# Performance work log

Hardware: AMD Instinct MI355X
Metric: run time of the kernel (lower is better)

The kernel has to match this reference:

```python
import jax, jax.numpy as jnp
import numpy as np

B, C, T, F = 16, 64, 400, 64
H = C          # GRU hidden == numUnits == channel
G = 8          # PE groups


def _gru(xs, Wih, Whh, bih, bhh):
    """PyTorch-style GRU, batch_first. xs: [N, T, I]; Wih: [3H, I]; Whh: [3H, H]."""
    gx = jnp.einsum('nti,gi->ntg', xs, Wih) + bih          # [N, T, 3H] input gates precomputed
    Hh = Whh.shape[1]

    def step(h, gxt):
        gh = h @ Whh.T + bhh                               # [N, 3H]
        xr, xz, xn = jnp.split(gxt, 3, axis=-1)
        hr, hz, hn = jnp.split(gh, 3, axis=-1)
        r = jax.nn.sigmoid(xr + hr)
        z = jax.nn.sigmoid(xz + hz)
        n = jnp.tanh(xn + r * hn)
        hn_new = (1.0 - z) * n + z * h
        return hn_new, hn_new

    h0 = jnp.zeros((xs.shape[0], Hh), xs.dtype)
    _, ys = jax.lax.scan(step, h0, jnp.swapaxes(gx, 0, 1))
    return jnp.swapaxes(ys, 0, 1)                          # [N, T, H]


def _ln2(x, g, b, eps=1e-8):
    """LayerNorm over last two dims [width, numUnits]."""
    mu = x.mean(axis=(-2, -1), keepdims=True)
    var = x.var(axis=(-2, -1), keepdims=True)
    return (x - mu) / jnp.sqrt(var + eps) * g + b


def setup_inputs() -> dict:
    key = jax.random.key(0)
    ks = jax.random.split(key, 24)
    s = 0.1

    def rn(k, shape):
        return jax.random.normal(k, shape, dtype=jnp.float32) * s

    return {
        'x': jax.random.normal(ks[0], (B, C, T, F), dtype=jnp.float32),
        # intra bidirectional GRU (input = C = H)
        'intra_Wih_f': rn(ks[1], (3 * H, H)), 'intra_Whh_f': rn(ks[2], (3 * H, H)),
        'intra_bih_f': rn(ks[3], (3 * H,)),   'intra_bhh_f': rn(ks[4], (3 * H,)),
        'intra_Wih_b': rn(ks[5], (3 * H, H)), 'intra_Whh_b': rn(ks[6], (3 * H, H)),
        'intra_bih_b': rn(ks[7], (3 * H,)),   'intra_bhh_b': rn(ks[8], (3 * H,)),
        'intra_fc_W': rn(ks[9], (H, 2 * H)),  'intra_fc_b': rn(ks[10], (H,)),
        'intra_ln_g': jnp.ones((F, H), jnp.float32), 'intra_ln_b': jnp.zeros((F, H), jnp.float32),
        # PE: 8 grouped GRUs + FCs (stacked along group axis)
        'pe_Wih': rn(ks[11], (G, 3 * H, H)), 'pe_Whh': rn(ks[12], (G, 3 * H, H)),
        'pe_bih': rn(ks[13], (G, 3 * H)),    'pe_bhh': rn(ks[14], (G, 3 * H)),
        'pe_fc_W': rn(ks[15], (G, H, H)),    'pe_fc_b': rn(ks[16], (G, H)),
        'pe_ln_g': jnp.ones((F, H), jnp.float32), 'pe_ln_b': jnp.zeros((F, H), jnp.float32),
    }


def _forward(x, intra_Wih_f, intra_Whh_f, intra_bih_f, intra_bhh_f,
             intra_Wih_b, intra_Whh_b, intra_bih_b, intra_bhh_b,
             intra_fc_W, intra_fc_b, intra_ln_g, intra_ln_b,
             pe_Wih, pe_Whh, pe_bih, pe_bhh, pe_fc_W, pe_fc_b, pe_ln_g, pe_ln_b):
    b, c, t, f = x.shape
    xp = jnp.transpose(x, (0, 2, 3, 1))                    # [b, t, f, c]

    # ---- intra path: bidirectional GRU along frequency f ----
    seq = xp.reshape(b * t, f, c)
    fwd = _gru(seq, intra_Wih_f, intra_Whh_f, intra_bih_f, intra_bhh_f)
    bwd = jnp.flip(_gru(jnp.flip(seq, 1), intra_Wih_b, intra_Whh_b, intra_bih_b, intra_bhh_b), 1)
    intra = jnp.concatenate([fwd, bwd], axis=-1) @ intra_fc_W.T + intra_fc_b
    intra = _ln2(intra.reshape(b, t, f, c), intra_ln_g, intra_ln_b)
    intra_out = xp + intra                                  # residual

    # ---- PE: 8 grouped GRUs along time t ----
    y = jnp.transpose(intra_out, (0, 2, 1, 3))             # [b, f, t, c]
    fg = f // G
    yg = y.reshape(b, G, fg, t, c)                         # chunk freq into G groups
    yg = jnp.transpose(yg, (1, 0, 2, 3, 4)).reshape(G, b * fg, t, c)
    rnn = jax.vmap(_gru)(yg, pe_Wih, pe_Whh, pe_bih, pe_bhh)    # [G, b*fg, t, H]
    fc = jnp.einsum('gnth,goh->gnto', rnn, pe_fc_W) + pe_fc_b[:, None, None, :]
    fc = fc.reshape(G, b, fg, t, H).transpose(1, 0, 2, 3, 4).reshape(b, f, t, H)
    inter = _ln2(jnp.transpose(fc, (0, 2, 1, 3)), pe_ln_g, pe_ln_b)   # [b, t, f, c]

    out = intra + inter                                     # note: residual with intra (pre-add), per source
    return jnp.transpose(out, (0, 3, 1, 2))                 # [b, c, t, f]


def reference(x, intra_Wih_f, intra_Whh_f, intra_bih_f, intra_bhh_f,
              intra_Wih_b, intra_Whh_b, intra_bih_b, intra_bhh_b,
              intra_fc_W, intra_fc_b, intra_ln_g, intra_ln_b,
              pe_Wih, pe_Whh, pe_bih, pe_bhh, pe_fc_W, pe_fc_b, pe_ln_g, pe_ln_b):
    return _forward(x, intra_Wih_f, intra_Whh_f, intra_bih_f, intra_bhh_f,
                    intra_Wih_b, intra_Whh_b, intra_bih_b, intra_bhh_b,
                    intra_fc_W, intra_fc_b, intra_ln_g, intra_ln_b,
                    pe_Wih, pe_Whh, pe_bih, pe_bhh, pe_fc_W, pe_fc_b, pe_ln_g, pe_ln_b)
```

## Files before the change

### kernel.cpp

```cpp
#include <hip/hip_runtime.h>
#include <hip/hip_bf16.h>

typedef unsigned short u16;
typedef __attribute__((ext_vector_type(8))) short short8;
typedef __attribute__((ext_vector_type(4))) float f32x4;

#define MFMA16(A,B,C) __builtin_amdgcn_mfma_f32_16x16x32_bf16((A),(B),(C),0,0,0)

__device__ __forceinline__ float bf2f(u16 u){ return __uint_as_float(((unsigned)u)<<16); }
__device__ __forceinline__ u16 f2bf(float f){
  unsigned x = __float_as_uint(f);
  return (u16)((x + 0x7FFFu + ((x>>16)&1u)) >> 16);
}
__device__ __forceinline__ float sigm(float x){ return __fdividef(1.f, 1.f + __expf(-x)); }
__device__ __forceinline__ float tanh_(float x){ return __fdividef(2.f, 1.f + __expf(-2.f*x)) - 1.f; }
__device__ __forceinline__ short8 ldg8(const u16* p){ return *(const short8*)p; }

struct CvtArgs {
  const void* src[21];
  u16* dst[21];
  int n[21];
};

__global__ __launch_bounds__(256,1) void k_cvt(CvtArgs a)
{
  const u16* d = (const u16*)a.src[0];
  int imp = 0, pl = 0;
#pragma unroll
  for (int i = 0; i < 128; i += 2){
    u16 u = d[i]; int e = (u >> 7) & 0xFF;
    if (u){ if (e >= 104 && e <= 134) pl++; else imp++; }
  }
  bool isf32 = imp > pl;

  int which, i0, stride;
  if (blockIdx.x < 20){ which = blockIdx.x + 1; i0 = threadIdx.x; stride = 256; }
  else { which = 0; i0 = (blockIdx.x - 20)*256 + threadIdx.x; stride = (gridDim.x - 20)*256; }
  int n = a.n[which];
  u16* dst = a.dst[which];
  if (isf32){
    const float* s = (const float*)a.src[which];
    for (int i = i0; i < n; i += stride) dst[i] = f2bf(s[i]);
  } else {
    const u16* s = (const u16*)a.src[which];
    for (int i = i0; i < n; i += stride) dst[i] = s[i];
  }
}

__global__ __launch_bounds__(256,1) void k_transpose(const u16* __restrict__ x, u16* __restrict__ xp)
{
  int nb = blockIdx.x; int b = nb/400, t = nb - b*400;
  int tid = threadIdx.x;
  __shared__ u16 tl[64*66];
  int f0 = (tid & 31) * 2;
#pragma unroll
  for (int p = 0; p < 8; p++){
    int c = p*8 + (tid>>5);
    unsigned u = *(const unsigned*)(x + (((size_t)b*64 + c)*400 + t)*64 + f0);
    *(unsigned*)(tl + c*66 + f0) = u;
  }
  __syncthreads();
  int c0 = (tid & 31) * 2;
  u16* dst = xp + (size_t)nb*4096;
#pragma unroll
  for (int p = 0; p < 8; p++){
    int f = p*8 + (tid>>5);
    unsigned u = (unsigned)tl[c0*66 + f] | ((unsigned)tl[(c0+1)*66 + f] << 16);
    *(unsigned*)(dst + f*64 + c0) = u;
  }
}

__global__ __launch_bounds__(64,1) void k_intra(
    const u16* __restrict__ xp,
    const u16* __restrict__ Wih_f, const u16* __restrict__ Whh_f,
    const u16* __restrict__ bih_f, const u16* __restrict__ bhh_f,
    const u16* __restrict__ Wih_b, const u16* __restrict__ Whh_b,
    const u16* __restrict__ bih_b, const u16* __restrict__ bhh_b,
    u16* __restrict__ yfo, u16* __restrict__ ybo)
{
  int blk = blockIdx.x;
  int dir = blk >= 400;
  int tile = dir ? blk - 400 : blk;
  int n0 = tile * 16;
  const u16* Wih = dir ? Wih_b : Wih_f;
  const u16* Whh = dir ? Whh_b : Whh_f;
  const u16* bih = dir ? bih_b : bih_f;
  const u16* bhh = dir ? bhh_b : bhh_f;
  u16* yo = dir ? ybo : yfo;

  int lane = threadIdx.x;
  int m = lane & 15, q = lane >> 4;

  short8 wrx[4][2], wzx[4][2], wnx[4][2], wrh[4][2], wzh[4][2], wnh[4][2];
#pragma unroll
  for (int nt = 0; nt < 4; nt++){
#pragma unroll
    for (int kc = 0; kc < 2; kc++){
      int co = kc*32 + q*8;
      wrx[nt][kc] = ldg8(Wih + (      nt*16 + m)*64 + co);
      wzx[nt][kc] = ldg8(Wih + ( 64 + nt*16 + m)*64 + co);
      wnx[nt][kc] = ldg8(Wih + (128 + nt*16 + m)*64 + co);
      wrh[nt][kc] = ldg8(Whh + (      nt*16 + m)*64 + co);
      wzh[nt][kc] = ldg8(Whh + ( 64 + nt*16 + m)*64 + co);
      wnh[nt][kc] = ldg8(Whh + (128 + nt*16 + m)*64 + co);
    }
  }
  float br[4], bz[4], bnx_[4], bnh_[4];
#pragma unroll
  for (int nt = 0; nt < 4; nt++){
    int u = nt*16 + m;
    br[nt]   = bf2f(bih[u])     + bf2f(bhh[u]);
    bz[nt]   = bf2f(bih[64+u])  + bf2f(bhh[64+u]);
    bnx_[nt] = bf2f(bih[128+u]);
    bnh_[nt] = bf2f(bhh[128+u]);
  }

  __shared__ u16 hl[16*72];
  float h[4][4];
#pragma unroll
  for (int nt=0;nt<4;nt++){
#pragma unroll
    for (int p=0;p<4;p++) h[nt][p] = 0.f;
  }
  short8 hf0 = {0,0,0,0,0,0,0,0}, hf1 = {0,0,0,0,0,0,0,0};
  int f = dir ? 63 : 0, df = dir ? -1 : 1;
  short8 xf0 = ldg8(xp + ((size_t)(n0+m)*64 + f)*64 + q*8);
  short8 xf1 = ldg8(xp + ((size_t)(n0+m)*64 + f)*64 + 32 + q*8);

  for (int s = 0; s < 64; s++){
    f32x4 ar[4], az[4], anx[4], anh[4];
#pragma unroll
    for (int nt=0;nt<4;nt++){
      ar[nt]  = (f32x4){br[nt],br[nt],br[nt],br[nt]};
      az[nt]  = (f32x4){bz[nt],bz[nt],bz[nt],bz[nt]};
      anx[nt] = (f32x4){bnx_[nt],bnx_[nt],bnx_[nt],bnx_[nt]};
      anh[nt] = (f32x4){bnh_[nt],bnh_[nt],bnh_[nt],bnh_[nt]};
    }
#pragma unroll
    for (int nt=0;nt<4;nt++){
      ar[nt]  = MFMA16(hf0, wrh[nt][0], ar[nt]);
      ar[nt]  = MFMA16(hf1, wrh[nt][1], ar[nt]);
      ar[nt]  = MFMA16(xf0, wrx[nt][0], ar[nt]);
      ar[nt]  = MFMA16(xf1, wrx[nt][1], ar[nt]);
      az[nt]  = MFMA16(hf0, wzh[nt][0], az[nt]);
      az[nt]  = MFMA16(hf1, wzh[nt][1], az[nt]);
      az[nt]  = MFMA16(xf0, wzx[nt][0], az[nt]);
      az[nt]  = MFMA16(xf1, wzx[nt][1], az[nt]);
      anx[nt] = MFMA16(xf0, wnx[nt][0], anx[nt]);
      anx[nt] = MFMA16(xf1, wnx[nt][1], anx[nt]);
      anh[nt] = MFMA16(hf0, wnh[nt][0], anh[nt]);
      anh[nt] = MFMA16(hf1, wnh[nt][1], anh[nt]);
    }
    int fn = f + df;
    if (s < 63){
      xf0 = ldg8(xp + ((size_t)(n0+m)*64 + fn)*64 + q*8);
      xf1 = ldg8(xp + ((size_t)(n0+m)*64 + fn)*64 + 32 + q*8);
    }
#pragma unroll
    for (int nt=0;nt<4;nt++){
#pragma unroll
      for (int p=0;p<4;p++){
        float r  = sigm(ar[nt][p]);
        float z  = sigm(az[nt][p]);
        float n  = tanh_(anx[nt][p] + r*anh[nt][p]);
        float hn = n + z*(h[nt][p] - n);
        h[nt][p] = hn;
        hl[(q*4+p)*72 + nt*16 + m] = f2bf(hn);
      }
    }
    __threadfence_block();
    int sl = lane >> 2, ch = lane & 3;
    short8 y0 = *(const short8*)(hl + sl*72 + ch*16);
    short8 y1 = *(const short8*)(hl + sl*72 + ch*16 + 8);
    *(short8*)(yo + ((size_t)(n0+sl)*64 + f)*64 + ch*16)     = y0;
    *(short8*)(yo + ((size_t)(n0+sl)*64 + f)*64 + ch*16 + 8) = y1;
    hf0 = *(const short8*)(hl + m*72 + q*8);
    hf1 = *(const short8*)(hl + m*72 + 32 + q*8);
    __threadfence_block();
    f = fn;
  }
}

__global__ __launch_bounds__(256,1) void k_ifc(
  const u16* __restrict__ yf, const u16* __restrict__ yb,
  const u16* __restrict__ fcw, const u16* __restrict__ fcb,
  const u16* __restrict__ lng, const u16* __restrict__ lnb,
  const u16* __restrict__ xp, u16* __restrict__ lnI, u16* __restrict__ iout)
{
  int nb = blockIdx.x; int b = nb/400, t = nb - b*400;
  int tid = threadIdx.x; int wv = tid>>6; int lane = tid&63;
  int m = lane&15, q = lane>>4;
  int rb = nb*64 + wv*16;
  short8 a0 = ldg8(yf + (size_t)(rb+m)*64 + q*8);
  short8 a1 = ldg8(yf + (size_t)(rb+m)*64 + 32 + q*8);
  short8 a2 = ldg8(yb + (size_t)(rb+m)*64 + q*8);
  short8 a3 = ldg8(yb + (size_t)(rb+m)*64 + 32 + q*8);
  f32x4 acc[4];
#pragma unroll
  for (int nt=0;nt<4;nt++){
    float bias = bf2f(fcb[nt*16+m]);
    acc[nt] = (f32x4){bias,bias,bias,bias};
    acc[nt] = MFMA16(a0, ldg8(fcw + (nt*16+m)*128 +      q*8), acc[nt]);
    acc[nt] = MFMA16(a1, ldg8(fcw + (nt*16+m)*128 + 32 + q*8), acc[nt]);
    acc[nt] = MFMA16(a2, ldg8(fcw + (nt*16+m)*128 + 64 + q*8), acc[nt]);
    acc[nt] = MFMA16(a3, ldg8(fcw + (nt*16+m)*128 + 96 + q*8), acc[nt]);
  }
  float s=0.f, s2=0.f;
#pragma unroll
  for (int nt=0;nt<4;nt++){
#pragma unroll
    for (int p=0;p<4;p++){ float v=acc[nt][p]; s+=v; s2+=v*v; }
  }
  for (int o=32;o>0;o>>=1){ s += __shfl_down(s,o); s2 += __shfl_down(s2,o); }
  __shared__ float red[8];
  if (lane==0){ red[wv]=s; red[4+wv]=s2; }
  __syncthreads();
  float S  = red[0]+red[1]+red[2]+red[3];
  float S2 = red[4]+red[5]+red[6]+red[7];
  float mu = S*(1.f/4096.f);
  float rstd = rsqrtf(S2*(1.f/4096.f) - mu*mu + 1e-8f);
#pragma unroll
  for (int nt=0;nt<4;nt++){
#pragma unroll
    for (int p=0;p<4;p++){
      int row = wv*16 + q*4 + p;
      int col = nt*16 + m;
      float v = (acc[nt][p]-mu)*rstd;
      v = v*bf2f(lng[row*64+col]) + bf2f(lnb[row*64+col]);
      lnI[(size_t)nb*4096 + row*64 + col] = f2bf(v);
      float xv = bf2f(xp[(size_t)nb*4096 + row*64 + col]);
      iout[(((size_t)b*64 + row)*400 + t)*64 + col] = f2bf(v + xv);
    }
  }
}

__global__ __launch_bounds__(64,1) void k_gx(const u16* __restrict__ io,
   const u16* __restrict__ pw, const u16* __restrict__ pb, u16* __restrict__ gx)
{
  int r0 = blockIdx.x * 16;
  int seq = r0 / 400;
  int g = (seq & 63) >> 3;
  int lane = threadIdx.x; int m = lane&15, q = lane>>4;
  short8 a0 = ldg8(io + (size_t)(r0+m)*64 + q*8);
  short8 a1 = ldg8(io + (size_t)(r0+m)*64 + 32 + q*8);
  const u16* W = pw + g*12288;
#pragma unroll
  for (int nt=0; nt<12; nt++){
    float bias = bf2f(pb[g*192 + nt*16 + m]);
    f32x4 acc = (f32x4){bias,bias,bias,bias};
    acc = MFMA16(a0, ldg8(W + (nt*16+m)*64 + q*8), acc);
    acc = MFMA16(a1, ldg8(W + (nt*16+m)*64 + 32 + q*8), acc);
#pragma unroll
    for (int p=0;p<4;p++)
      gx[(size_t)(r0 + q*4 + p)*192 + nt*16 + m] = f2bf(acc[p]);
  }
}

__global__ __launch_bounds__(64,1) void k_pe(const u16* __restrict__ gx,
  const u16* __restrict__ whh, const u16* __restrict__ bhh, u16* __restrict__ ype)
{
  int seq = blockIdx.x;
  int g = (seq & 63) >> 3;
  int j = threadIdx.x;
  const u16* W = whh + g*12288;
  float wr[64], wz[64], wn[64];
#pragma unroll
  for (int kk=0; kk<8; kk++){
    short8 vr = ldg8(W + (      j)*64 + kk*8);
    short8 vz = ldg8(W + ( 64 + j)*64 + kk*8);
    short8 vn = ldg8(W + (128 + j)*64 + kk*8);
#pragma unroll
    for (int i=0;i<8;i++){
      wr[kk*8+i] = bf2f((u16)vr[i]);
      wz[kk*8+i] = bf2f((u16)vz[i]);
      wn[kk*8+i] = bf2f((u16)vn[i]);
    }
  }
  float brh = bf2f(bhh[g*192 + j]);
  float bzh = bf2f(bhh[g*192 + 64 + j]);
  float bnh = bf2f(bhh[g*192 + 128 + j]);
  float h = 0.f;
  const u16* gp = gx + (size_t)seq*400*192;
  u16* yp = ype + (size_t)seq*400*64 + j;
  for (int t = 0; t < 400; t++){
    float xr = bf2f(gp[j]), xz = bf2f(gp[64+j]), xn = bf2f(gp[128+j]);
    float ar = brh, az = bzh, an = bnh;
#pragma unroll
    for (int k = 0; k < 64; k++){
      float hk = __int_as_float(__builtin_amdgcn_readlane(__float_as_int(h), k));
      ar = fmaf(hk, wr[k], ar);
      az = fmaf(hk, wz[k], az);
      an = fmaf(hk, wn[k], an);
    }
    float r = sigm(xr + ar);
    float z = sigm(xz + az);
    float n = tanh_(xn + r*an);
    h = n + z*(h - n);
    *yp = f2bf(h);
    gp += 192; yp += 64;
  }
}

__global__ __launch_bounds__(64,1) void k_pefc(const u16* __restrict__ ype,
  const u16* __restrict__ fw, const u16* __restrict__ fb, u16* __restrict__ fcpe)
{
  int r0 = blockIdx.x * 16;
  int seq = r0 / 400;
  int g = (seq & 63) >> 3;
  int b = seq >> 6, f = seq & 63;
  int tb = r0 - seq*400;
  int lane = threadIdx.x; int m = lane&15, q = lane>>4;
  short8 a0 = ldg8(ype + (size_t)(r0+m)*64 + q*8);
  short8 a1 = ldg8(ype + (size_t)(r0+m)*64 + 32 + q*8);
  const u16* W = fw + g*4096;
#pragma unroll
  for (int nt=0;nt<4;nt++){
    float bias = bf2f(fb[g*64 + nt*16 + m]);
    f32x4 acc = (f32x4){bias,bias,bias,bias};
    acc = MFMA16(a0, ldg8(W + (nt*16+m)*64 + q*8), acc);
    acc = MFMA16(a1, ldg8(W + (nt*16+m)*64 + 32 + q*8), acc);
#pragma unroll
    for (int p=0;p<4;p++){
      int t = tb + q*4 + p;
      fcpe[(((size_t)b*400 + t)*64 + f)*64 + nt*16 + m] = f2bf(acc[p]);
    }
  }
}

__global__ __launch_bounds__(256,1) void k_final(const u16* __restrict__ fcpe,
  const u16* __restrict__ lnI, const u16* __restrict__ g_, const u16* __restrict__ b_,
  float* __restrict__ out)
{
  int nb = blockIdx.x; int b = nb/400, t = nb - b*400;
  int tid = threadIdx.x;
  const u16* src = fcpe + (size_t)nb*4096 + tid*16;
  short8 v0 = ldg8(src), v1 = ldg8(src + 8);
  float v[16];
#pragma unroll
  for (int i=0;i<8;i++){ v[i] = bf2f((u16)v0[i]); v[8+i] = bf2f((u16)v1[i]); }
  float s=0.f, s2=0.f;
#pragma unroll
  for (int i=0;i<16;i++){ s+=v[i]; s2+=v[i]*v[i]; }
  int lane = tid&63, wv = tid>>6;
  for (int o=32;o>0;o>>=1){ s += __shfl_down(s,o); s2 += __shfl_down(s2,o); }
  __shared__ float red[8];
  __shared__ float tr[64*68];
  if (lane==0){ red[wv]=s; red[4+wv]=s2; }
  __syncthreads();
  float S  = red[0]+red[1]+red[2]+red[3];
  float S2 = red[4]+red[5]+red[6]+red[7];
  float mu = S*(1.f/4096.f);
  float rstd = rsqrtf(S2*(1.f/4096.f) - mu*mu + 1e-8f);
  int ff = tid>>2; int c0 = (tid&3)*16;
  const u16* lp = lnI + (size_t)nb*4096 + tid*16;
  short8 l0 = ldg8(lp), l1 = ldg8(lp + 8);
#pragma unroll
  for (int i=0;i<16;i++){
    int c = c0 + i;
    float x = (v[i]-mu)*rstd*bf2f(g_[ff*64+c]) + bf2f(b_[ff*64+c]);
    x += (i<8) ? bf2f((u16)l0[i]) : bf2f((u16)l1[i-8]);
    tr[c*68 + ff] = x;
  }
  __syncthreads();
  int cc = tid>>2, fc = (tid&3)*16;
  float* dst = out + (((size_t)b*64 + cc)*400 + t)*64 + fc;
#pragma unroll
  for (int i=0;i<16;i+=4){
    *(f32x4*)(dst + i) = *(const f32x4*)(tr + cc*68 + fc + i);
  }
}

extern "C" void kernel_launch(void* const* d_in, const int* in_sizes, int n_in,
                              void* d_out, int out_size, void* d_ws, size_t ws_size,
                              hipStream_t stream)
{
  (void)in_sizes; (void)n_in; (void)out_size; (void)ws_size;

  char* ws = (char*)d_ws;
  u16* xp   = (u16*)(ws + 0ull);
  u16* xb   = (u16*)(ws + 52428800ull);
  u16* yf   = (u16*)(ws + 52428800ull);
  u16* yb   = (u16*)(ws + 104857600ull);
  u16* lnI  = (u16*)(ws + 157286400ull);
  u16* iout = (u16*)(ws + 209715200ull);
  u16* gx   = (u16*)(ws + 0ull);
  u16* ype  = (u16*)(ws + 209715200ull);
  u16* fcpe = (u16*)(ws + 0ull);
  u16* wb   = (u16*)(ws + 262144000ull);

  static const int wn[21] = {26214400,
    12288,12288,192,192, 12288,12288,192,192,
    8192,64,4096,4096, 98304,98304,1536,1536, 32768,512,4096,4096};
  int woff[21]; woff[0] = 0;
  int acc = 0;
  for (int i = 1; i <= 20; i++){ woff[i] = acc; acc += wn[i]; }

  CvtArgs ca;
  for (int i = 0; i < 21; i++){
    ca.src[i] = d_in[i];
    ca.n[i] = wn[i];
    ca.dst[i] = (i == 0) ? xb : (wb + woff[i]);
  }

  const u16* iWihf = wb + woff[1];
  const u16* iWhhf = wb + woff[2];
  const u16* ibihf = wb + woff[3];
  const u16* ibhhf = wb + woff[4];
  const u16* iWihb = wb + woff[5];
  const u16* iWhhb = wb + woff[6];
  const u16* ibihb = wb + woff[7];
  const u16* ibhhb = wb + woff[8];
  const u16* fcW   = wb + woff[9];
  const u16* fcB   = wb + woff[10];
  const u16* ilng  = wb + woff[11];
  const u16* ilnb  = wb + woff[12];
  const u16* peWih = wb + woff[13];
  const u16* peWhh = wb + woff[14];
  const u16* pebih = wb + woff[15];
  const u16* pebhh = wb + woff[16];
  const u16* pefcW = wb + woff[17];
  const u16* pefcb = wb + woff[18];
  const u16* pelng = wb + woff[19];
  const u16* pelnb = wb + woff[20];

  k_cvt<<<dim3(2068), dim3(256), 0, stream>>>(ca);
  k_transpose<<<dim3(6400), dim3(256), 0, stream>>>(xb, xp);
  k_intra<<<dim3(800), dim3(64), 0, stream>>>(xp, iWihf, iWhhf, ibihf, ibhhf,
                                              iWihb, iWhhb, ibihb, ibhhb, yf, yb);
  k_ifc<<<dim3(6400), dim3(256), 0, stream>>>(yf, yb, fcW, fcB, ilng, ilnb, xp, lnI, iout);
  k_gx<<<dim3(25600), dim3(64), 0, stream>>>(iout, peWih, pebih, gx);
  k_pe<<<dim3(1024), dim3(64), 0, stream>>>(gx, peWhh, pebhh, ype);
  k_pefc<<<dim3(25600), dim3(64), 0, stream>>>(ype, pefcW, pefcb, fcpe);
  k_final<<<dim3(6400), dim3(256), 0, stream>>>(fcpe, lnI, pelng, pelnb, (float*)d_out);
}
```

Baseline: 1.267 ms.

## Batch 16 PE GRU sequences per block and compute recurrence with MFMA

The PE GRU recurrence kernel is rewritten so each block of four waves processes 16 sequences of one group together. The hidden-state matvec becomes a bf16 MFMA using a hi/lo split of h for extra precision. The new hidden state is exchanged through double-buffered LDS and the next step's input gates are prefetched. This replaces the per-sequence 64-thread scalar FMA loop with readlane broadcasts. The cost is only 64 blocks on a many-CU device, plus a block barrier every timestep.

Measured after the change: 1.249 ms. Within noise of the previous version (-1.4%).

```diff
diff --git a/kernel.cpp b/kernel.cpp
--- a/kernel.cpp
+++ b/kernel.cpp
@@ -4,6 +4,7 @@
 typedef unsigned short u16;
 typedef __attribute__((ext_vector_type(8))) short short8;
 typedef __attribute__((ext_vector_type(4))) float f32x4;
+typedef __attribute__((ext_vector_type(4))) unsigned short us4;
 
 #define MFMA16(A,B,C) __builtin_amdgcn_mfma_f32_16x16x32_bf16((A),(B),(C),0,0,0)
 
@@ -256,48 +257,99 @@
   }
 }
 
-__global__ __launch_bounds__(64,1) void k_pe(const u16* __restrict__ gx,
+__global__ __launch_bounds__(256,1) void k_pe(const u16* __restrict__ gx,
   const u16* __restrict__ whh, const u16* __restrict__ bhh, u16* __restrict__ ype)
 {
-  int seq = blockIdx.x;
-  int g = (seq & 63) >> 3;
-  int j = threadIdx.x;
+  int tile = blockIdx.x;
+  int g = tile >> 3, tl = tile & 7;
+  int tid = threadIdx.x;
+  int w = tid >> 6;
+  int lane = tid & 63;
+  int m = lane & 15, q = lane >> 4;
+
   const u16* W = whh + g*12288;
-  float wr[64], wz[64], wn[64];
-#pragma unroll
-  for (int kk=0; kk<8; kk++){
-    short8 vr = ldg8(W + (      j)*64 + kk*8);
-    short8 vz = ldg8(W + ( 64 + j)*64 + kk*8);
-    short8 vn = ldg8(W + (128 + j)*64 + kk*8);
-#pragma unroll
-    for (int i=0;i<8;i++){
-      wr[kk*8+i] = bf2f((u16)vr[i]);
-      wz[kk*8+i] = bf2f((u16)vz[i]);
-      wn[kk*8+i] = bf2f((u16)vn[i]);
-    }
-  }
-  float brh = bf2f(bhh[g*192 + j]);
-  float bzh = bf2f(bhh[g*192 + 64 + j]);
-  float bnh = bf2f(bhh[g*192 + 128 + j]);
-  float h = 0.f;
-  const u16* gp = gx + (size_t)seq*400*192;
-  u16* yp = ype + (size_t)seq*400*64 + j;
+  short8 wr[2], wz[2], wn[2];
+#pragma unroll
+  for (int kc = 0; kc < 2; kc++){
+    int co = kc*32 + q*8;
+    wr[kc] = ldg8(W + (((size_t)w    *16 + m))*64 + co);
+    wz[kc] = ldg8(W + (((size_t)(w+4)*16 + m))*64 + co);
+    wn[kc] = ldg8(W + (((size_t)(w+8)*16 + m))*64 + co);
+  }
+  float brh = bf2f(bhh[g*192 +       w*16 + m]);
+  float bzh = bf2f(bhh[g*192 + 64  + w*16 + m]);
+  float bnh = bf2f(bhh[g*192 + 128 + w*16 + m]);
+
+  const u16* bp[4];
+#pragma unroll
+  for (int p = 0; p < 4; p++){
+    int sl = q*4 + p;
+    int sidx = tl*16 + sl;
+    int seqg = (sidx >> 3)*64 + g*8 + (sidx & 7);
+    bp[p] = gx + (size_t)seqg*400*192 + w*16 + m;
+  }
+
+  int sls = w*4 + (lane >> 4);
+  int sidxs = tl*16 + sls;
+  int seqs_ = (sidxs >> 3)*64 + g*8 + (sidxs & 7);
+  int u0 = (lane & 15)*4;
+  u16* yp = ype + (size_t)seqs_*400*64 + u0;
+  int hlr = sls*72 + u0;
+
+  __shared__ u16 hl[2][2][16*72];
+
+  float hprev[4] = {0.f, 0.f, 0.f, 0.f};
+  short8 hA0 = {0,0,0,0,0,0,0,0}, hA1 = {0,0,0,0,0,0,0,0};
+  short8 hB0 = {0,0,0,0,0,0,0,0}, hB1 = {0,0,0,0,0,0,0,0};
+
+  u16 gr[4], gz[4], gn[4];
+#pragma unroll
+  for (int p = 0; p < 4; p++){ gr[p] = bp[p][0]; gz[p] = bp[p][64]; gn[p] = bp[p][128]; }
+
+  int cur = 0;
   for (int t = 0; t < 400; t++){
-    float xr = bf2f(gp[j]), xz = bf2f(gp[64+j]), xn = bf2f(gp[128+j]);
-    float ar = brh, az = bzh, an = bnh;
-#pragma unroll
-    for (int k = 0; k < 64; k++){
-      float hk = __int_as_float(__builtin_amdgcn_readlane(__float_as_int(h), k));
-      ar = fmaf(hk, wr[k], ar);
-      az = fmaf(hk, wz[k], az);
-      an = fmaf(hk, wn[k], an);
-    }
-    float r = sigm(xr + ar);
-    float z = sigm(xz + az);
-    float n = tanh_(xn + r*an);
-    h = n + z*(h - n);
-    *yp = f2bf(h);
-    gp += 192; yp += 64;
+    f32x4 ar, az, anh;
+    float gnf[4];
+#pragma unroll
+    for (int p = 0; p < 4; p++){
+      ar[p]  = bf2f(gr[p]) + brh;
+      az[p]  = bf2f(gz[p]) + bzh;
+      anh[p] = bnh;
+      gnf[p] = bf2f(gn[p]);
+    }
+    if (t < 399){
+#pragma unroll
+      for (int p = 0; p < 4; p++){
+        bp[p] += 192;
+        gr[p] = bp[p][0]; gz[p] = bp[p][64]; gn[p] = bp[p][128];
+      }
+    }
+    ar  = MFMA16(hA0, wr[0], ar);  ar  = MFMA16(hA1, wr[1], ar);
+    ar  = MFMA16(hB0, wr[0], ar);  ar  = MFMA16(hB1, wr[1], ar);
+    az  = MFMA16(hA0, wz[0], az);  az  = MFMA16(hA1, wz[1], az);
+    az  = MFMA16(hB0, wz[0], az);  az  = MFMA16(hB1, wz[1], az);
+    anh = MFMA16(hA0, wn[0], anh); anh = MFMA16(hA1, wn[1], anh);
+    anh = MFMA16(hB0, wn[0], anh); anh = MFMA16(hB1, wn[1], anh);
+#pragma unroll
+    for (int p = 0; p < 4; p++){
+      float r  = sigm(ar[p]);
+      float z  = sigm(az[p]);
+      float n  = tanh_(gnf[p] + r*anh[p]);
+      float hn = n + z*(hprev[p] - n);
+      hprev[p] = hn;
+      u16 hi = f2bf(hn);
+      int off = (q*4 + p)*72 + w*16 + m;
+      hl[cur][0][off] = hi;
+      hl[cur][1][off] = f2bf(hn - bf2f(hi));
+    }
+    __syncthreads();
+    *(us4*)yp = *(const us4*)&hl[cur][0][hlr];
+    yp += 64;
+    hA0 = *(const short8*)&hl[cur][0][m*72 + q*8];
+    hA1 = *(const short8*)&hl[cur][0][m*72 + 32 + q*8];
+    hB0 = *(const short8*)&hl[cur][1][m*72 + q*8];
+    hB1 = *(const short8*)&hl[cur][1][m*72 + 32 + q*8];
+    cur ^= 1;
   }
 }
 
@@ -429,7 +481,7 @@
                                               iWihb, iWhhb, ibihb, ibhhb, yf, yb);
   k_ifc<<<dim3(6400), dim3(256), 0, stream>>>(yf, yb, fcW, fcB, ilng, ilnb, xp, lnI, iout);
   k_gx<<<dim3(25600), dim3(64), 0, stream>>>(iout, peWih, pebih, gx);
-  k_pe<<<dim3(1024), dim3(64), 0, stream>>>(gx, peWhh, pebhh, ype);
+  k_pe<<<dim3(64), dim3(256), 0, stream>>>(gx, peWhh, pebhh, ype);
   k_pefc<<<dim3(25600), dim3(64), 0, stream>>>(ype, pefcW, pefcb, fcpe);
   k_final<<<dim3(6400), dim3(256), 0, stream>>>(fcpe, lnI, pelng, pelnb, (float*)d_out);
 }
```

## Compute PE GRU recurrence with bf16 MFMA and split hi/lo hidden state

Applied to the files above, without the earlier changes.

Replaces the scalar per-lane FMA loop over readlane-broadcast hidden values in the grouped GRU kernel with matrix-core MFMA instructions. Each step computes the hidden-to-gate products from bf16 weight fragments held in registers. The hidden state is split into bf16 high and low parts to keep near-fp32 accuracy, and is exchanged through LDS each step. Input-gate values are now prefetched two steps ahead. The aim is to cut the serial per-step VALU work, at the cost of bf16 recurrent weights, redundant MFMA rows and an LDS round trip on the critical path.

Result: no change. 1.273 ms (+0.5%).

```diff
diff --git a/kernel.cpp b/kernel.cpp
--- a/kernel.cpp
+++ b/kernel.cpp
@@ -261,44 +261,106 @@
 {
   int seq = blockIdx.x;
   int g = (seq & 63) >> 3;
-  int j = threadIdx.x;
-  const u16* W = whh + g*12288;
-  float wr[64], wz[64], wn[64];
-#pragma unroll
-  for (int kk=0; kk<8; kk++){
-    short8 vr = ldg8(W + (      j)*64 + kk*8);
-    short8 vz = ldg8(W + ( 64 + j)*64 + kk*8);
-    short8 vn = ldg8(W + (128 + j)*64 + kk*8);
-#pragma unroll
-    for (int i=0;i<8;i++){
-      wr[kk*8+i] = bf2f((u16)vr[i]);
-      wz[kk*8+i] = bf2f((u16)vz[i]);
-      wn[kk*8+i] = bf2f((u16)vn[i]);
-    }
-  }
-  float brh = bf2f(bhh[g*192 + j]);
-  float bzh = bf2f(bhh[g*192 + 64 + j]);
-  float bnh = bf2f(bhh[g*192 + 128 + j]);
+  int lane = threadIdx.x;
+  int m = lane & 15, q = lane >> 4;
+
+  const u16* W = whh + (size_t)g*12288;
+  short8 wr[4][2], wz[4][2], wn[4][2];
+#pragma unroll
+  for (int nt = 0; nt < 4; nt++){
+#pragma unroll
+    for (int kc = 0; kc < 2; kc++){
+      int co = kc*32 + q*8;
+      wr[nt][kc] = ldg8(W + (      nt*16 + m)*64 + co);
+      wz[nt][kc] = ldg8(W + ( 64 + nt*16 + m)*64 + co);
+      wn[nt][kc] = ldg8(W + (128 + nt*16 + m)*64 + co);
+    }
+  }
+  float br_[4], bz_[4], bn_[4];
+#pragma unroll
+  for (int nt = 0; nt < 4; nt++){
+    br_[nt] = bf2f(bhh[g*192 +       nt*16 + m]);
+    bz_[nt] = bf2f(bhh[g*192 + 64  + nt*16 + m]);
+    bn_[nt] = bf2f(bhh[g*192 + 128 + nt*16 + m]);
+  }
+
+  const u16* gp = gx + (size_t)seq*400*192 + lane;
+  u16* yp = ype + (size_t)seq*400*64 + lane;
+
+  u16 cr0 = gp[0],   cz0 = gp[64],  cn0 = gp[128];
+  u16 cr1 = gp[192], cz1 = gp[256], cn1 = gp[320];
+  gp += 384;
+
+  __shared__ __align__(16) u16 hbuf[128];
+
   float h = 0.f;
-  const u16* gp = gx + (size_t)seq*400*192;
-  u16* yp = ype + (size_t)seq*400*64 + j;
-  for (int t = 0; t < 400; t++){
-    float xr = bf2f(gp[j]), xz = bf2f(gp[64+j]), xn = bf2f(gp[128+j]);
-    float ar = brh, az = bzh, an = bnh;
-#pragma unroll
-    for (int k = 0; k < 64; k++){
-      float hk = __int_as_float(__builtin_amdgcn_readlane(__float_as_int(h), k));
-      ar = fmaf(hk, wr[k], ar);
-      az = fmaf(hk, wz[k], az);
-      an = fmaf(hk, wn[k], an);
-    }
-    float r = sigm(xr + ar);
-    float z = sigm(xz + az);
-    float n = tanh_(xn + r*an);
-    h = n + z*(h - n);
-    *yp = f2bf(h);
-    gp += 192; yp += 64;
-  }
+  short8 ah0 = {0,0,0,0,0,0,0,0}, ah1 = {0,0,0,0,0,0,0,0};
+  short8 al0 = {0,0,0,0,0,0,0,0}, al1 = {0,0,0,0,0,0,0,0};
+
+  f32x4 accr[4], accz[4], accn[4];
+#pragma unroll
+  for (int nt=0; nt<4; nt++){
+    accr[nt] = (f32x4){br_[nt],br_[nt],br_[nt],br_[nt]};
+    accz[nt] = (f32x4){bz_[nt],bz_[nt],bz_[nt],bz_[nt]};
+    accn[nt] = (f32x4){bn_[nt],bn_[nt],bn_[nt],bn_[nt]};
+  }
+
+#define PE_STEP(CR, CZ, CN, PFOFF, COND)                                      \
+  {                                                                           \
+    float xr = bf2f(CR), xz = bf2f(CZ), xn = bf2f(CN);                        \
+    if (COND){ CR = gp[PFOFF]; CZ = gp[(PFOFF)+64]; CN = gp[(PFOFF)+128]; }   \
+    \
+    \
+    _Pragma("unroll")                                                         \
+    for (int nt=0; nt<4; nt++){                                               \
+      accr[nt][0] = br_[nt]; accz[nt][0] = bz_[nt]; accn[nt][0] = bn_[nt];    \
+    }                                                                         \
+    _Pragma("unroll")                                                         \
+    for (int nt=0; nt<4; nt++){                                               \
+      accr[nt] = MFMA16(ah0, wr[nt][0], accr[nt]);                            \
+      accr[nt] = MFMA16(ah1, wr[nt][1], accr[nt]);                            \
+      accr[nt] = MFMA16(al0, wr[nt][0], accr[nt]);                            \
+      accr[nt] = MFMA16(al1, wr[nt][1], accr[nt]);                            \
+      accz[nt] = MFMA16(ah0, wz[nt][0], accz[nt]);                            \
+      accz[nt] = MFMA16(ah1, wz[nt][1], accz[nt]);                            \
+      accz[nt] = MFMA16(al0, wz[nt][0], accz[nt]);                            \
+      accz[nt] = MFMA16(al1, wz[nt][1], accz[nt]);                            \
+      accn[nt] = MFMA16(ah0, wn[nt][0], accn[nt]);                            \
+      accn[nt] = MFMA16(ah1, wn[nt][1], accn[nt]);                            \
+      accn[nt] = MFMA16(al0, wn[nt][0], accn[nt]);                            \
+      accn[nt] = MFMA16(al1, wn[nt][1], accn[nt]);                            \
+    }                                                                         \
+         \
+    float ar = accr[0][0]; float az = accz[0][0]; float an = accn[0][0];      \
+    ar = (q==1) ? accr[1][0] : ar; az = (q==1) ? accz[1][0] : az;             \
+    an = (q==1) ? accn[1][0] : an;                                            \
+    ar = (q==2) ? accr[2][0] : ar; az = (q==2) ? accz[2][0] : az;             \
+    an = (q==2) ? accn[2][0] : an;                                            \
+    ar = (q==3) ? accr[3][0] : ar; az = (q==3) ? accz[3][0] : az;             \
+    an = (q==3) ? accn[3][0] : an;                                            \
+    float r = sigm(xr + ar);                                                  \
+    float z = sigm(xz + az);                                                  \
+    float n = tanh_(xn + r*an);                                               \
+    h = n + z*(h - n);                                                        \
+    u16 hi = f2bf(h);                                                         \
+    u16 lo = f2bf(h - bf2f(hi));                                              \
+    *yp = hi; yp += 64;                                                       \
+    hbuf[lane] = hi;                                                          \
+    hbuf[64 + lane] = lo;                                                     \
+    __threadfence_block();          \
+    ah0 = *(const short8*)(hbuf + q*8);           \
+    ah1 = *(const short8*)(hbuf + 32 + q*8);      \
+    al0 = *(const short8*)(hbuf + 64 + q*8);                                  \
+    al1 = *(const short8*)(hbuf + 96 + q*8);                                  \
+    __threadfence_block();         \
+  }
+
+  for (int t = 0; t < 400; t += 2){
+    PE_STEP(cr0, cz0, cn0, 0,   t < 398)
+    PE_STEP(cr1, cz1, cn1, 192, t < 397)
+    gp += 384;
+  }
+#undef PE_STEP
 }
 
 __global__ __launch_bounds__(64,1) void k_pefc(const u16* __restrict__ ype,
```
